# Performance work log

Hardware: AMD Instinct MI355X
Metric: run time of the kernel (lower is better)

## Reference

```python
import jax, jax.numpy as jnp
import numpy as np
from jax import lax

KS = 16          # kernel_size
VAR_WEIGHT = 1.0
VAR_BIAS = 0.1


def setup_inputs() -> dict:
    key = jax.random.key(0)
    k1, k2 = jax.random.split(key)
    N1, N2, C, W, H = 128, 128, 512, 16, 16
    x = jax.random.normal(k1, (N1, C, W, H), dtype=jnp.float32)
    y = jax.random.normal(k2, (N2, C, W, H), dtype=jnp.float32)
    # Conv2d buffer: box kernel scaled by var_weight / kernel_size**2
    kernel = jnp.ones((1, 1, KS, KS), dtype=jnp.float32) * (VAR_WEIGHT / KS ** 2)
    return {"x": x, "y": y, "kernel": kernel}


def _box_conv(patch, kernel):
    # patch: [N, 1, W, H]; padding=0, stride=1, dilation=1 -> VALID, full-spatial
    out = lax.conv_general_dilated(
        patch, kernel,
        window_strides=(1, 1), padding="VALID",
        dimension_numbers=("NCHW", "OIHW", "NCHW"))
    return out + VAR_BIAS


def reference(x, y, kernel):
    N1, C, W, H = x.shape
    N2 = y.shape[0]
    # Fused correlation volume: mean over channels of the outer product,
    # computed as a batched GEMM per spatial location (no N1*N2*C*W*H blowup).
    xy = jnp.einsum("icwh,jcwh->ijwh", x, y) / C          # [N1, N2, W, H]
    xy = xy.reshape(N1 * N2, 1, W, H)
    # Box-filter conv collapses spatial dims (kernel_size == W == H, padding=0).
    r = _box_conv(xy, kernel)                              # [N1*N2, 1, 1, 1]
    # Note: original also convolves xx/yy, but NonlinKP(final_kp).xy only
    # uses the xy branch for the returned value.
    return r.reshape(N1, N2)
```

## Files before the change

### kernel.cpp

```cpp
#include <hip/hip_runtime.h>
#include <hip/hip_bf16.h>

typedef short s16x8 __attribute__((ext_vector_type(8)));
typedef float f32x4 __attribute__((ext_vector_type(4)));

#define M_DIM   128
#define K_DIM   131072
#define NSPLIT  512
#define KC      (K_DIM / NSPLIT)
#define BK      64
#define NSTEP   (KC / BK)
#define THREADS 512
#define OUT_N   (M_DIM * M_DIM)

__device__ __forceinline__ short f2bf(float f) {
    unsigned u = __builtin_bit_cast(unsigned, f);
    u += 0x7fffu + ((u >> 16) & 1u);
    return (short)(u >> 16);
}
__device__ __forceinline__ float bf2f(unsigned short h) {
    unsigned u = ((unsigned)h) << 16;
    return __builtin_bit_cast(float, u);
}

__device__ __forceinline__ s16x8 cvt8(float4 a, float4 b) {
    s16x8 r;
    r[0] = f2bf(a.x); r[1] = f2bf(a.y); r[2] = f2bf(a.z); r[3] = f2bf(a.w);
    r[4] = f2bf(b.x); r[5] = f2bf(b.y); r[6] = f2bf(b.z); r[7] = f2bf(b.w);
    return r;
}

__global__ __launch_bounds__(THREADS) void gemm_splitk(
    const float* __restrict__ x, const float* __restrict__ y,
    const float* __restrict__ kern,
    unsigned short* __restrict__ ws, float* __restrict__ out, int use_ws)
{
    __shared__ __align__(16) short lds[2][2][M_DIM][BK];

    const int t    = threadIdx.x;
    const long kb0 = (long)blockIdx.x * KC;

    const int srow = t >> 3;
    const int sg   = t & 7;
    const int wofs = (sg ^ (srow & 7)) * 8;

    const float* xa = x + (size_t)srow        * K_DIM + kb0 + sg * 8;
    const float* xb = x + (size_t)(srow + 64) * K_DIM + kb0 + sg * 8;
    const float* ya = y + (size_t)srow        * K_DIM + kb0 + sg * 8;
    const float* yb = y + (size_t)(srow + 64) * K_DIM + kb0 + sg * 8;

    const int wave = t >> 6;
    const int lane = t & 63;
    const int wr   = wave >> 2;
    const int wc   = wave & 3;
    const int l15  = lane & 15;
    const int l4   = lane >> 4;

    f32x4 acc[4][2] = {};
    float4 r0, r1, r2, r3, r4, r5, r6, r7;

    auto stage_load = [&](long kb) {
        r0 = *(const float4*)(xa + kb); r1 = *(const float4*)(xa + kb + 4);
        r2 = *(const float4*)(xb + kb); r3 = *(const float4*)(xb + kb + 4);
        r4 = *(const float4*)(ya + kb); r5 = *(const float4*)(ya + kb + 4);
        r6 = *(const float4*)(yb + kb); r7 = *(const float4*)(yb + kb + 4);
    };
    auto stage_write = [&](int buf) {
        *(s16x8*)&lds[buf][0][srow     ][wofs] = cvt8(r0, r1);
        *(s16x8*)&lds[buf][0][srow + 64][wofs] = cvt8(r2, r3);
        *(s16x8*)&lds[buf][1][srow     ][wofs] = cvt8(r4, r5);
        *(s16x8*)&lds[buf][1][srow + 64][wofs] = cvt8(r6, r7);
    };
    auto compute = [&](int buf) {
        #pragma unroll
        for (int ks = 0; ks < 2; ++ks) {
            s16x8 af[4], bf[2];
            const int g = ks * 4 + l4;
            #pragma unroll
            for (int m = 0; m < 4; ++m) {
                const int row = wr * 64 + m * 16 + l15;
                af[m] = *(const s16x8*)&lds[buf][0][row][(g ^ (row & 7)) * 8];
            }
            #pragma unroll
            for (int n = 0; n < 2; ++n) {
                const int row = wc * 32 + n * 16 + l15;
                bf[n] = *(const s16x8*)&lds[buf][1][row][(g ^ (row & 7)) * 8];
            }
            #pragma unroll
            for (int m = 0; m < 4; ++m)
                #pragma unroll
                for (int n = 0; n < 2; ++n)
                    acc[m][n] = __builtin_amdgcn_mfma_f32_16x16x32_bf16(
                        af[m], bf[n], acc[m][n], 0, 0, 0);
        }
    };

    stage_load(0);
    stage_write(0);
    __syncthreads();

    for (int s = 0; s < NSTEP; ++s) {
        const int buf = s & 1;
        if (s + 1 < NSTEP) {
            stage_load((long)(s + 1) * BK);
            compute(buf);
            stage_write(buf ^ 1);
            __syncthreads();
        } else {
            compute(buf);
        }
    }

    if (use_ws) {
        unsigned short* wp = ws + (size_t)blockIdx.x * OUT_N;
        #pragma unroll
        for (int m = 0; m < 4; ++m) {
            const int row = wr * 64 + m * 16 + l4 * 4;
            #pragma unroll
            for (int n = 0; n < 2; ++n) {
                const int col = wc * 32 + n * 16 + l15;
                #pragma unroll
                for (int r = 0; r < 4; ++r)
                    wp[(size_t)(row + r) * M_DIM + col] =
                        (unsigned short)f2bf(acc[m][n][r]);
            }
        }
    } else {
        const float scale = kern[0] * (1.0f / 512.0f);
        #pragma unroll
        for (int m = 0; m < 4; ++m) {
            const int row = wr * 64 + m * 16 + l4 * 4;
            #pragma unroll
            for (int n = 0; n < 2; ++n) {
                const int col = wc * 32 + n * 16 + l15;
                #pragma unroll
                for (int r = 0; r < 4; ++r)
                    atomicAdd(out + (size_t)(row + r) * M_DIM + col,
                              acc[m][n][r] * scale);
            }
        }
    }
}

__global__ __launch_bounds__(256) void reduce_k(
    const unsigned short* __restrict__ ws, const float* __restrict__ kern,
    float* __restrict__ out)
{
    __shared__ float red[16][16][4];
    const int b  = blockIdx.x;
    const int qi = threadIdx.x & 15;
    const int sc = threadIdx.x >> 4;
    const int e0 = b * 64 + qi * 4;

    float a0 = 0.f, a1 = 0.f, a2 = 0.f, a3 = 0.f;
    #pragma unroll 4
    for (int s = sc * 32; s < sc * 32 + 32; ++s) {
        ushort4 v = *(const ushort4*)(ws + (size_t)s * OUT_N + e0);
        a0 += bf2f(v.x); a1 += bf2f(v.y); a2 += bf2f(v.z); a3 += bf2f(v.w);
    }
    red[sc][qi][0] = a0; red[sc][qi][1] = a1;
    red[sc][qi][2] = a2; red[sc][qi][3] = a3;
    __syncthreads();
    for (int off = 8; off > 0; off >>= 1) {
        if (sc < off) {
            #pragma unroll
            for (int r = 0; r < 4; ++r)
                red[sc][qi][r] += red[sc + off][qi][r];
        }
        __syncthreads();
    }
    if (sc == 0) {
        const float scale = kern[0] * (1.0f / 512.0f);
        float4 o;
        o.x = red[0][qi][0] * scale + 0.1f;
        o.y = red[0][qi][1] * scale + 0.1f;
        o.z = red[0][qi][2] * scale + 0.1f;
        o.w = red[0][qi][3] * scale + 0.1f;
        *(float4*)(out + e0) = o;
    }
}

__global__ __launch_bounds__(256) void init_k(float* __restrict__ out) {
    out[blockIdx.x * 256 + threadIdx.x] = 0.1f;
}

extern "C" void kernel_launch(void* const* d_in, const int* in_sizes, int n_in,
                              void* d_out, int out_size, void* d_ws, size_t ws_size,
                              hipStream_t stream) {
    const float* x    = (const float*)d_in[0];
    const float* y    = (const float*)d_in[1];
    const float* kern = (const float*)d_in[2];
    float* out = (float*)d_out;

    const size_t need = (size_t)NSPLIT * OUT_N * sizeof(unsigned short);
    if (ws_size >= need && d_ws != nullptr) {
        unsigned short* ws = (unsigned short*)d_ws;
        gemm_splitk<<<NSPLIT, THREADS, 0, stream>>>(x, y, kern, ws, out, 1);
        reduce_k<<<256, 256, 0, stream>>>(ws, kern, out);
    } else {
        init_k<<<OUT_N / 256, 256, 0, stream>>>(out);
        gemm_splitk<<<NSPLIT, THREADS, 0, stream>>>(x, y, kern, nullptr, out, 0);
    }
}
```

Measured before the change: 32.63 us.

## Halve split-K count and prefetch two stages ahead with dual register sets

Reduces the split-K factor from 512 to 256, so each block covers twice as much K and the bf16 workspace traffic and reduction work are halved. The main loop is restructured to hold two register stages (A and B), issuing global loads two steps ahead and unrolling by two with fixed LDS buffers. This aims to hide global load latency better and cut the partial-sum write and read cost. In exchange it doubles staging register usage and launches only 256 blocks, which may underfill the GPU's compute units.

```diff
diff --git a/kernel.cpp b/kernel.cpp
--- a/kernel.cpp
+++ b/kernel.cpp
@@ -6,7 +6,7 @@
 
 #define M_DIM   128
 #define K_DIM   131072
-#define NSPLIT  512
+#define NSPLIT  256
 #define KC      (K_DIM / NSPLIT)
 #define BK      64
 #define NSTEP   (KC / BK)
@@ -22,7 +22,6 @@
     unsigned u = ((unsigned)h) << 16;
     return __builtin_bit_cast(float, u);
 }
-
 __device__ __forceinline__ s16x8 cvt8(float4 a, float4 b) {
     s16x8 r;
     r[0] = f2bf(a.x); r[1] = f2bf(a.y); r[2] = f2bf(a.z); r[3] = f2bf(a.w);
@@ -57,20 +56,22 @@
     const int l4   = lane >> 4;
 
     f32x4 acc[4][2] = {};
-    float4 r0, r1, r2, r3, r4, r5, r6, r7;
-
-    auto stage_load = [&](long kb) {
-        r0 = *(const float4*)(xa + kb); r1 = *(const float4*)(xa + kb + 4);
-        r2 = *(const float4*)(xb + kb); r3 = *(const float4*)(xb + kb + 4);
-        r4 = *(const float4*)(ya + kb); r5 = *(const float4*)(ya + kb + 4);
-        r6 = *(const float4*)(yb + kb); r7 = *(const float4*)(yb + kb + 4);
-    };
-    auto stage_write = [&](int buf) {
-        *(s16x8*)&lds[buf][0][srow     ][wofs] = cvt8(r0, r1);
-        *(s16x8*)&lds[buf][0][srow + 64][wofs] = cvt8(r2, r3);
-        *(s16x8*)&lds[buf][1][srow     ][wofs] = cvt8(r4, r5);
-        *(s16x8*)&lds[buf][1][srow + 64][wofs] = cvt8(r6, r7);
-    };
+
+    float4 A0,A1,A2,A3,A4,A5,A6,A7;
+    float4 B0,B1,B2,B3,B4,B5,B6,B7;
+
+    #define STAGE_LOAD(R, kb)                                            \
+        R##0 = *(const float4*)(xa + (kb)); R##1 = *(const float4*)(xa + (kb) + 4); \
+        R##2 = *(const float4*)(xb + (kb)); R##3 = *(const float4*)(xb + (kb) + 4); \
+        R##4 = *(const float4*)(ya + (kb)); R##5 = *(const float4*)(ya + (kb) + 4); \
+        R##6 = *(const float4*)(yb + (kb)); R##7 = *(const float4*)(yb + (kb) + 4);
+
+    #define STAGE_WRITE(R, buf)                                          \
+        *(s16x8*)&lds[buf][0][srow     ][wofs] = cvt8(R##0, R##1);       \
+        *(s16x8*)&lds[buf][0][srow + 64][wofs] = cvt8(R##2, R##3);       \
+        *(s16x8*)&lds[buf][1][srow     ][wofs] = cvt8(R##4, R##5);       \
+        *(s16x8*)&lds[buf][1][srow + 64][wofs] = cvt8(R##6, R##7);
+
     auto compute = [&](int buf) {
         #pragma unroll
         for (int ks = 0; ks < 2; ++ks) {
@@ -95,20 +96,21 @@
         }
     };
 
-    stage_load(0);
-    stage_write(0);
+    STAGE_LOAD(A, 0)
+    STAGE_LOAD(B, BK)
+    STAGE_WRITE(A, 0)
     __syncthreads();
 
-    for (int s = 0; s < NSTEP; ++s) {
-        const int buf = s & 1;
-        if (s + 1 < NSTEP) {
-            stage_load((long)(s + 1) * BK);
-            compute(buf);
-            stage_write(buf ^ 1);
-            __syncthreads();
-        } else {
-            compute(buf);
-        }
+    #pragma unroll
+    for (int s = 0; s < NSTEP; s += 2) {
+        if (s + 2 < NSTEP) { STAGE_LOAD(A, (long)(s + 2) * BK) }
+        compute(0);
+        STAGE_WRITE(B, 1)
+        __syncthreads();
+        if (s + 3 < NSTEP) { STAGE_LOAD(B, (long)(s + 3) * BK) }
+        compute(1);
+        if (s + 2 < NSTEP) { STAGE_WRITE(A, 0) }
+        __syncthreads();
     }
 
     if (use_ws) {
@@ -140,6 +142,8 @@
             }
         }
     }
+    #undef STAGE_LOAD
+    #undef STAGE_WRITE
 }
 
 __global__ __launch_bounds__(256) void reduce_k(
@@ -154,7 +158,7 @@
 
     float a0 = 0.f, a1 = 0.f, a2 = 0.f, a3 = 0.f;
     #pragma unroll 4
-    for (int s = sc * 32; s < sc * 32 + 32; ++s) {
+    for (int s = sc * 16; s < sc * 16 + 16; ++s) {
         ushort4 v = *(const ushort4*)(ws + (size_t)s * OUT_N + e0);
         a0 += bf2f(v.x); a1 += bf2f(v.y); a2 += bf2f(v.z); a3 += bf2f(v.w);
     }
```

After: 29.77 us. -8.8%, faster.
